# Kernel optimization log

Hardware: AMD Instinct MI355X
Metric: run time of the kernel (lower is better)

Reference implementation:

```python
import jax, jax.numpy as jnp
import numpy as np

N, E = 100000, 1600000
IN_CH, HID, HEADS, OUT_CH = 128, 32, 2, 40
NEG_SLOPE = 0.2
BN_EPS = 1e-5


def _param(key, shape, scale=0.1):
    return scale * jax.random.normal(key, shape, dtype=jnp.float32)


def setup_inputs() -> dict:
    key = jax.random.key(0)
    ks = jax.random.split(key, 24)
    x = jax.random.normal(ks[0], (N, IN_CH), dtype=jnp.float32)
    edge_index = jax.random.randint(ks[1], (2, E), 0, N, dtype=jnp.int32)
    d0 = HEADS * HID  # 64
    inp = {
        'x': x, 'edge_index': edge_index,
        # conv0: in 128 -> 32 per head, concat -> 64
        'W0': _param(ks[2], (IN_CH, HEADS * HID)),
        'as0': _param(ks[3], (HEADS, HID)), 'ad0': _param(ks[4], (HEADS, HID)),
        'b0': jnp.zeros((d0,), jnp.float32),
        'g0': jnp.ones((d0,), jnp.float32), 'bt0': jnp.zeros((d0,), jnp.float32),
        # conv1: 64 -> 32 per head, concat -> 64
        'W1': _param(ks[5], (d0, HEADS * HID)),
        'as1': _param(ks[6], (HEADS, HID)), 'ad1': _param(ks[7], (HEADS, HID)),
        'b1': jnp.zeros((d0,), jnp.float32),
        'g1': jnp.ones((d0,), jnp.float32), 'bt1': jnp.zeros((d0,), jnp.float32),
        # conv2: 64 -> 40 per head, mean over heads -> 40
        'W2': _param(ks[8], (d0, HEADS * OUT_CH)),
        'as2': _param(ks[9], (HEADS, OUT_CH)), 'ad2': _param(ks[10], (HEADS, OUT_CH)),
        'b2': jnp.zeros((OUT_CH,), jnp.float32),
    }
    return inp


def gat_conv(x, src, dst, W, a_src, a_dst, bias, out_ch, concat):
    n = x.shape[0]
    h = (x @ W).reshape(n, HEADS, out_ch)            # [N,H,C]
    alpha_src = jnp.sum(h * a_src, axis=-1)          # [N,H]
    alpha_dst = jnp.sum(h * a_dst, axis=-1)          # [N,H]
    e = jax.nn.leaky_relu(alpha_src[src] + alpha_dst[dst], NEG_SLOPE)  # [E,H]
    # softmax over incoming edges per destination node (self loops guarantee >=1 edge)
    m = jax.ops.segment_max(e, dst, num_segments=n)
    e = jnp.exp(e - m[dst])
    s = jax.ops.segment_sum(e, dst, num_segments=n)
    alpha = e / s[dst]                                # [E,H]
    msg = h[src] * alpha[:, :, None]                  # [E,H,C]
    out = jax.ops.segment_sum(msg, dst, num_segments=n)  # [N,H,C]
    out = out.reshape(n, HEADS * out_ch) if concat else out.mean(axis=1)
    return out + bias


def batch_norm(x, gamma, beta):
    mu = jnp.mean(x, axis=0)
    var = jnp.mean(jnp.square(x - mu), axis=0)
    return gamma * (x - mu) * jax.lax.rsqrt(var + BN_EPS) + beta


def reference(x, edge_index, W0, as0, ad0, b0, g0, bt0,
              W1, as1, ad1, b1, g1, bt1, W2, as2, ad2, b2):
    n = x.shape[0]
    loops = jnp.arange(n, dtype=edge_index.dtype)
    src = jnp.concatenate([edge_index[0], loops])
    dst = jnp.concatenate([edge_index[1], loops])
    h = gat_conv(x, src, dst, W0, as0, ad0, b0, HID, True)
    h = jax.nn.elu(batch_norm(h, g0, bt0))
    h = gat_conv(h, src, dst, W1, as1, ad1, b1, HID, True)
    h = jax.nn.elu(batch_norm(h, g1, bt1))
    return gat_conv(h, src, dst, W2, as2, ad2, b2, OUT_CH, False)
```

## Files before the change

### kernel.cpp

```cpp
#include <hip/hip_runtime.h>
#include <hip/hip_bf16.h>
#include <math.h>


#define NNODES 100000
#define NEDGES 1600000
#define ENTOT  (NEDGES + NNODES)
#define NEG_SLOPE 0.2f
#define BN_EPS 1e-5f

#define NRANGE 8
#define RSIZE  (NNODES/NRANGE)
#define BCAP   262144
#define PBLK   2048
#define NB2    32

typedef unsigned short u16;
typedef unsigned int u32;
typedef unsigned long long u64;
typedef __attribute__((ext_vector_type(8))) short short8;
typedef __attribute__((ext_vector_type(4))) float f32x4;

__device__ __forceinline__ float b2f(u16 u){ union{u32 i; float f;} v; v.i=((u32)u)<<16; return v.f; }
__device__ __forceinline__ float blo(u32 u){ union{u32 i; float f;} v; v.i=u<<16; return v.f; }
__device__ __forceinline__ float bhi(u32 u){ union{u32 i; float f;} v; v.i=u&0xffff0000u; return v.f; }
__device__ __forceinline__ u16 f2b(float x){ __hip_bfloat16 b=__float2bfloat16(x); return *(u16*)&b; }
__device__ __forceinline__ float ldf(const void* p, int i, int f){
  return f ? ((const float*)p)[i] : b2f(((const u16*)p)[i]);
}

__global__ void k_detect(const u16* __restrict__ x, int* __restrict__ flag){
  __shared__ int bad;
  if(threadIdx.x==0) bad=0;
  __syncthreads();
  int cnt=0;
  for(int i=threadIdx.x;i<4096;i+=256){
    u16 v = x[2*i];
    int ex = (v>>7)&0xff;
    if(ex==0xff || (ex==0 && (v&0x7fff)!=0)) cnt++;
  }
  atomicAdd(&bad,cnt);
  __syncthreads();
  if(threadIdx.x==0) flag[0] = (bad>4)?1:0;
}

__global__ __launch_bounds__(256) void k_part2(
    const int* __restrict__ ei, int* __restrict__ gptr, u32* __restrict__ bkt){
  __shared__ int lcnt[NRANGE], gbase[NRANGE];
  int t=threadIdx.x;
  if(t<NRANGE) lcnt[t]=0;
  __syncthreads();
  const int CH=(ENTOT+PBLK-1)/PBLK;
  int beg=blockIdx.x*CH, end=beg+CH; if(end>ENTOT) end=ENTOT;
  int nd[4], ns[4], nr[4], ne=0;
  for(int i=beg+t; i<end; i+=256){
    int d=(i<NEDGES)? ei[NEDGES+i] : (i-NEDGES);
    int s=(i<NEDGES)? ei[i] : d;
    nd[ne]=d; ns[ne]=s; ne++;
  }
  #pragma unroll 4
  for(int k=0;k<ne;k++) nr[k]=atomicAdd(&lcnt[nd[k]/RSIZE],1);
  __syncthreads();
  if(t<NRANGE) gbase[t]=atomicAdd(&gptr[t],lcnt[t]);
  __syncthreads();
  #pragma unroll 4
  for(int k=0;k<ne;k++){
    int r=nd[k]/RSIZE;
    u32 e = ((u32)(nd[k]-r*RSIZE)<<17) | (u32)ns[k];
    __builtin_nontemporal_store(e, &bkt[(size_t)r*BCAP + gbase[r] + nr[k]]);
  }
}

__global__ __launch_bounds__(256) void k_hist4(
    const u32* __restrict__ bkt, const int* __restrict__ gptr, int* __restrict__ lhist){
  __shared__ int lh[RSIZE];
  int t=threadIdx.x;
  for(int i=t;i<RSIZE;i+=256) lh[i]=0;
  __syncthreads();
  int r = blockIdx.x & (NRANGE-1);
  int c = blockIdx.x >> 3;
  int n = gptr[r];
  int per=(n+NB2-1)/NB2;
  int beg=c*per, end=beg+per; if(end>n) end=n;
  const u32* bp = bkt + (size_t)r*BCAP;
  for(int i=beg+t;i<end;i+=256) atomicAdd(&lh[bp[i]>>17],1);
  __syncthreads();
  int* out = lhist + (size_t)(r*NB2+c)*RSIZE;
  for(int i=t;i<RSIZE;i+=256) out[i]=lh[i];
}

__global__ __launch_bounds__(256) void k_sumscan(int* __restrict__ lhist, int* __restrict__ cnt){
  int n = blockIdx.x*256 + threadIdx.x;
  if(n>=NNODES) return;
  int r = n/RSIZE, i = n - r*RSIZE;
  int* base = lhist + (size_t)r*NB2*RSIZE + i;
  int run=0;
  #pragma unroll 8
  for(int c=0;c<NB2;c++){
    int v = base[(size_t)c*RSIZE];
    base[(size_t)c*RSIZE] = run;
    run += v;
  }
  cnt[n]=run;
}

#define SCAN_M (NNODES+1)
#define SCAN_NB ((SCAN_M + 2047)/2048)

__global__ void k_scan_a(const int* __restrict__ cnt, int* __restrict__ bsum){
  __shared__ int red[256];
  int b=blockIdx.x, t=threadIdx.x;
  int base = b*2048 + t*8;
  int s=0;
  #pragma unroll
  for(int j=0;j<8;j++){ int idx=base+j; s += (idx<NNODES)? cnt[idx]:0; }
  red[t]=s; __syncthreads();
  for(int o=128;o>0;o>>=1){ if(t<o) red[t]+=red[t+o]; __syncthreads(); }
  if(t==0) bsum[b]=red[0];
}

__global__ void k_scan_b(int* bsum){
  if(threadIdx.x==0){
    int run=0;
    for(int i=0;i<SCAN_NB;i++){ int v=bsum[i]; bsum[i]=run; run+=v; }
  }
}

__global__ void k_scan_c(const int* __restrict__ cnt, const int* __restrict__ bsum,
                         int* __restrict__ row_ptr){
  __shared__ int lds[256];
  int b=blockIdx.x, t=threadIdx.x;
  int base=b*2048+t*8;
  int v[8]; int s=0;
  #pragma unroll
  for(int j=0;j<8;j++){ int idx=base+j; int x=(idx<NNODES)?cnt[idx]:0; v[j]=s; s+=x; }
  lds[t]=s; __syncthreads();
  for(int o=1;o<256;o<<=1){
    int other=0; if(t>=o) other=lds[t-o];
    __syncthreads();
    lds[t]+=other;
    __syncthreads();
  }
  int texcl = lds[t] - s;
  int off0 = bsum[b] + texcl;
  #pragma unroll
  for(int j=0;j<8;j++){ int idx=base+j; if(idx<SCAN_M) row_ptr[idx]=off0+v[j]; }
}

__global__ __launch_bounds__(256) void k_scatter4(
    const u32* __restrict__ bkt, const int* __restrict__ gptr,
    const int* __restrict__ row_ptr, const int* __restrict__ lhist,
    int* __restrict__ col){
  __shared__ int lofs[RSIZE];
  int t=threadIdx.x;
  int r = blockIdx.x & (NRANGE-1);
  int c = blockIdx.x >> 3;
  int lo = r*RSIZE;
  const int* cb = lhist + (size_t)(r*NB2+c)*RSIZE;
  for(int i=t;i<RSIZE;i+=256) lofs[i] = row_ptr[lo+i] + cb[i];
  __syncthreads();
  int n = gptr[r];
  int per=(n+NB2-1)/NB2;
  int beg=c*per, end=beg+per; if(end>n) end=n;
  const u32* bp = bkt + (size_t)r*BCAP;
  for(int i=beg+t;i<end;i+=256){
    u32 e=bp[i];
    int pos=atomicAdd(&lofs[e>>17],1);
    col[pos]=(int)(e & 0x1FFFF);
  }
}

template<int K, int OUTC, int HID, bool XEXT, bool BN>
__global__ __launch_bounds__(256) void k_gemm_mfma(
    const void* __restrict__ xin, const void* __restrict__ W,
    const void* __restrict__ avs, const void* __restrict__ avd,
    const float2* __restrict__ bnab,
    u16* __restrict__ hout, float* __restrict__ asrc, float* __restrict__ adst,
    const int* __restrict__ flagp)
{
  const int f = flagp[0];
  constexpr int KP = K+8;
  constexpr int RS = OUTC+8;
  constexpr int NT = OUTC/16;
  constexpr int KQ = K/32;
  __shared__ __align__(16) u16 WT[OUTC*KP];
  __shared__ __align__(16) u16 HROW[4*16*RS];
  __shared__ float AVb[2*OUTC];
  __shared__ float2 BB[K];
  int t=threadIdx.x;
  const u16* Wu=(const u16*)W; const float* Wf=(const float*)W;
  for(int i8=t*8; i8<K*OUTC; i8+=256*8){
    int k=i8/OUTC, c0=i8-k*OUTC;
    u16 w8[8];
    if(f){
      const float* wp=Wf+i8;
      float4 a=*(const float4*)wp, b=*(const float4*)(wp+4);
      w8[0]=f2b(a.x);w8[1]=f2b(a.y);w8[2]=f2b(a.z);w8[3]=f2b(a.w);
      w8[4]=f2b(b.x);w8[5]=f2b(b.y);w8[6]=f2b(b.z);w8[7]=f2b(b.w);
    } else {
      uint4 q=*(const uint4*)(Wu+i8);
      w8[0]=q.x&0xffff;w8[1]=q.x>>16;w8[2]=q.y&0xffff;w8[3]=q.y>>16;
      w8[4]=q.z&0xffff;w8[5]=q.z>>16;w8[6]=q.w&0xffff;w8[7]=q.w>>16;
    }
    #pragma unroll
    for(int u=0;u<8;u++) WT[(c0+u)*KP + k] = w8[u];
  }
  for(int idx=t; idx<2*OUTC; idx+=256)
    AVb[idx] = (idx<OUTC)? ldf(avs,idx,f) : ldf(avd,idx-OUTC,f);
  if(BN) for(int idx=t; idx<K; idx+=256) BB[idx]=bnab[idx];
  __syncthreads();

  int wv=t>>6, lane=t&63;
  int m=lane&15, quad=lane>>4;
  int grow0 = blockIdx.x*64 + wv*16;
  int growA = grow0 + m;
  bool avalid = growA < NNODES;
  int growC = avalid ? growA : 0;

  f32x4 acc[NT] = {};
  #pragma unroll
  for(int kq=0;kq<KQ;kq++){
    int k0 = kq*32 + quad*8;
    union{ u32 u[4]; short8 s8; } A;
    if(XEXT && f==1){
      const float* xr=(const float*)xin + (size_t)growC*K + k0;
      float4 p=*(const float4*)xr, q=*(const float4*)(xr+4);
      A.u[0]=f2b(p.x)|((u32)f2b(p.y)<<16);
      A.u[1]=f2b(p.z)|((u32)f2b(p.w)<<16);
      A.u[2]=f2b(q.x)|((u32)f2b(q.y)<<16);
      A.u[3]=f2b(q.z)|((u32)f2b(q.w)<<16);
    } else {
      uint4 q=*(const uint4*)((const u16*)xin + (size_t)growC*K + k0);
      A.u[0]=q.x; A.u[1]=q.y; A.u[2]=q.z; A.u[3]=q.w;
    }
    if(BN){
      #pragma unroll
      for(int j=0;j<4;j++){
        float lo=b2f(A.u[j]&0xffff), hi=b2f(A.u[j]>>16);
        float2 c1=BB[k0+2*j], c2=BB[k0+2*j+1];
        lo=c1.x*lo+c1.y; lo = lo>0.f? lo : __expf(lo)-1.f;
        hi=c2.x*hi+c2.y; hi = hi>0.f? hi : __expf(hi)-1.f;
        A.u[j]=f2b(lo)|((u32)f2b(hi)<<16);
      }
    }
    #pragma unroll
    for(int nt=0;nt<NT;nt++){
      union{ uint4 q; short8 s8; } Bf;
      Bf.q = *(const uint4*)&WT[(nt*16+m)*KP + k0];
      acc[nt] = __builtin_amdgcn_mfma_f32_16x16x32_bf16(A.s8, Bf.s8, acc[nt], 0,0,0);
    }
  }
  u16* hr = &HROW[wv*16*RS];
  #pragma unroll
  for(int nt=0;nt<NT;nt++){
    #pragma unroll
    for(int reg=0;reg<4;reg++)
      hr[(quad*4+reg)*RS + nt*16+m] = f2b(acc[nt][reg]);
  }
  __syncthreads();
  {
    int row=lane&15, task=quad, head=task&1, sd=task>>1;
    float p=0.f;
    const u16* hrow=&hr[row*RS + head*HID];
    const float* av=&AVb[sd*OUTC + head*HID];
    #pragma unroll 8
    for(int c=0;c<HID;c++) p += b2f(hrow[c])*av[c];
    int grow=grow0+row;
    if(grow<NNODES){ (sd? adst:asrc)[grow*2+head]=p; }
  }
  {
    constexpr int CH8 = OUTC/8;
    for(int idx=lane; idx<16*CH8; idx+=64){
      int rr=idx/CH8, c8=idx-rr*CH8;
      int grow=grow0+rr;
      if(grow<NNODES)
        *(uint4*)(hout + (size_t)grow*OUTC + c8*8) = *(const uint4*)&hr[rr*RS + c8*8];
    }
  }
}

template<int OUTC, bool FINAL>
__global__ __launch_bounds__(256) void k_aggf(
  const int* __restrict__ row_ptr, const int* __restrict__ col,
  const u16* __restrict__ hin, const float2* __restrict__ asrc2,
  const float2* __restrict__ adst2, const void* __restrict__ bias,
  u16* __restrict__ houtb, void* __restrict__ outv, const int* __restrict__ flagp)
{
  const int f = flagp[0];
  __shared__ float vbuf[FINAL?32:1][84];
  constexpr int HSPLIT = FINAL ? 5 : 4;
  int t = threadIdx.x;
  int g  = t>>3;
  int cg = t&7;
  int rr = blockIdx.x & 7, jb = blockIdx.x >> 3;
  int lim = RSIZE - jb*32;
  bool ok = g < lim;
  int d = rr*RSIZE + jb*32 + g;
  int base=0, deg=0;
  float2 adv = make_float2(0.f,0.f);
  if(ok){
    base = row_ptr[d];
    deg  = row_ptr[d+1] - base;
    adv  = adst2[d];
  }
  const int* cp  = col + base;
  const u16* hcg = hin + cg*8;
  const u16* hxg = hin + 64 + cg*2;
  float acc[8]={0,0,0,0,0,0,0,0}, accx0=0.f, accx1=0.f;
  float s0=0.f, s1=0.f;

  int    cA[4]={0,0,0,0}, cB[4]={0,0,0,0};
  float2 aA[4]={}, aB[4]={};
  uint4  hA[4]={}, hB[4]={};
  ushort2 xA[4]={}, xB[4]={};

#define LDBLK(JJ, C, A, H, X) do{ int lm_=deg-1; \
    C[0]=cp[((JJ)  <lm_)?(JJ)  :lm_]; C[1]=cp[((JJ)+1<lm_)?(JJ)+1:lm_]; \
    C[2]=cp[((JJ)+2<lm_)?(JJ)+2:lm_]; C[3]=cp[((JJ)+3<lm_)?(JJ)+3:lm_]; \
    A[0]=asrc2[C[0]]; A[1]=asrc2[C[1]]; A[2]=asrc2[C[2]]; A[3]=asrc2[C[3]]; \
    H[0]=*(const uint4*)(hcg+(size_t)C[0]*OUTC); \
    H[1]=*(const uint4*)(hcg+(size_t)C[1]*OUTC); \
    H[2]=*(const uint4*)(hcg+(size_t)C[2]*OUTC); \
    H[3]=*(const uint4*)(hcg+(size_t)C[3]*OUTC); \
    if(FINAL){ \
      X[0]=*(const ushort2*)(hxg+(size_t)C[0]*OUTC); \
      X[1]=*(const ushort2*)(hxg+(size_t)C[1]*OUTC); \
      X[2]=*(const ushort2*)(hxg+(size_t)C[2]*OUTC); \
      X[3]=*(const ushort2*)(hxg+(size_t)C[3]*OUTC); } \
  }while(0)

#define COMP4(J, A, H, X) do{ \
    _Pragma("unroll") \
    for(int k_=0;k_<4;k_++){ \
      bool vv = (J)+k_ < deg; \
      float e0=A[k_].x+adv.x; e0=fmaxf(e0,NEG_SLOPE*e0); e0=fminf(e0,60.f); \
      float e1=A[k_].y+adv.y; e1=fmaxf(e1,NEG_SLOPE*e1); e1=fminf(e1,60.f); \
      float p0=__expf(e0), p1=__expf(e1); \
      if(!vv){p0=0.f;p1=0.f;} \
      s0+=p0; s1+=p1; \
      float pc=(cg<HSPLIT)?p0:p1; \
      acc[0]+=pc*blo(H[k_].x); acc[1]+=pc*bhi(H[k_].x); \
      acc[2]+=pc*blo(H[k_].y); acc[3]+=pc*bhi(H[k_].y); \
      acc[4]+=pc*blo(H[k_].z); acc[5]+=pc*bhi(H[k_].z); \
      acc[6]+=pc*blo(H[k_].w); acc[7]+=pc*bhi(H[k_].w); \
      if(FINAL){ accx0+=p1*b2f(X[k_].x); accx1+=p1*b2f(X[k_].y); } \
    } \
  }while(0)

  if(deg>0) LDBLK(0, cA, aA, hA, xA);
  for(int j=0;j<deg;j+=4){
    if(j+4<deg) LDBLK(j+4, cB, aB, hB, xB);
    COMP4(j, aA, hA, xA);
    #pragma unroll
    for(int k_=0;k_<4;k_++){ cA[k_]=cB[k_]; aA[k_]=aB[k_]; hA[k_]=hB[k_]; }
    if(FINAL){
      #pragma unroll
      for(int k_=0;k_<4;k_++) xA[k_]=xB[k_];
    }
  }
#undef LDBLK
#undef COMP4

  float inv0 = s0>0.f?1.f/s0:0.f, inv1 = s1>0.f?1.f/s1:0.f;
  if(!FINAL){
    if(ok){
      float inv = (cg<4)? inv0 : inv1;
      u16 o8[8];
      #pragma unroll
      for(int k=0;k<8;k++) o8[k]=f2b(acc[k]*inv + ldf(bias,cg*8+k,f));
      uint4 ov;
      ov.x=(u32)o8[0]|((u32)o8[1]<<16); ov.y=(u32)o8[2]|((u32)o8[3]<<16);
      ov.z=(u32)o8[4]|((u32)o8[5]<<16); ov.w=(u32)o8[6]|((u32)o8[7]<<16);
      *(uint4*)(houtb + (size_t)d*64 + cg*8) = ov;
    }
  } else {
    if(ok){
      #pragma unroll
      for(int k=0;k<8;k++)
        vbuf[g][cg*8+k] = acc[k]*((cg<5)?inv0:inv1);
      vbuf[g][64+cg*2]   = accx0*inv1;
      vbuf[g][64+cg*2+1] = accx1*inv1;
    }
    __syncthreads();
    for(int idx=t; idx<32*40; idx+=256){
      int gg=idx/40, ch=idx-gg*40;
      if(gg<lim){
        int dd = rr*RSIZE + jb*32 + gg;
        float res = 0.5f*(vbuf[gg][ch] + vbuf[gg][40+ch]) + ldf(bias,ch,f);
        if(f) ((float*)outv)[(size_t)dd*40+ch] = res;
        else  ((__hip_bfloat16*)outv)[(size_t)dd*40+ch] = __float2bfloat16(res);
      }
    }
  }
}

__global__ __launch_bounds__(256) void k_bnstats(const u16* __restrict__ h, float* __restrict__ stats){
  __shared__ float red[4][128];
  int t=threadIdx.x; int c=t&63; int g=t>>6;
  float s=0.f,q=0.f;
  for(int r=blockIdx.x*4+g; r<NNODES; r+=gridDim.x*4){
    float v=b2f(h[(size_t)r*64+c]); s+=v; q+=v*v;
  }
  red[g][c]=s; red[g][64+c]=q;
  __syncthreads();
  if(t<128){
    float tot=red[0][t]+red[1][t]+red[2][t]+red[3][t];
    atomicAdd(&stats[t], tot);
  }
}

__global__ void k_bnfinal(const float* __restrict__ stats,
                          const void* __restrict__ gm, const void* __restrict__ bt,
                          float2* __restrict__ bnab, const int* __restrict__ flagp){
  const int f = flagp[0];
  int c=threadIdx.x;
  if(c>=64) return;
  float mu=stats[c]*(1.0f/NNODES);
  float var=stats[64+c]*(1.0f/NNODES)-mu*mu;
  var = var>0.f?var:0.f;
  float A = ldf(gm,c,f)*rsqrtf(var+BN_EPS);
  float B = ldf(bt,c,f) - A*mu;
  bnab[c]=make_float2(A,B);
}

extern "C" void kernel_launch(void* const* d_in, const int* in_sizes, int n_in,
                              void* d_out, int out_size, void* d_ws, size_t ws_size,
                              hipStream_t stream){
  const void* x  =d_in[0];
  const int* ei =(const int*)d_in[1];
  const void* W0 =d_in[2];  const void* as0=d_in[3];  const void* ad0=d_in[4];
  const void* b0 =d_in[5];  const void* g0 =d_in[6];  const void* bt0=d_in[7];
  const void* W1 =d_in[8];  const void* as1=d_in[9];  const void* ad1=d_in[10];
  const void* b1 =d_in[11]; const void* g1 =d_in[12]; const void* bt1=d_in[13];
  const void* W2 =d_in[14]; const void* as2=d_in[15]; const void* ad2=d_in[16];
  const void* b2 =d_in[17];

  char* ws=(char*)d_ws;
  size_t off=0;
  auto alloc=[&](size_t bytes)->void*{ void* p=ws+off; off+=(bytes+255)&~(size_t)255; return p; };
  int*    flag   =(int*)   alloc(256);
  int*    row_ptr=(int*)   alloc((size_t)(NNODES+1)*4);
  int*    cnt    =(int*)   alloc((size_t)NNODES*4);
  int*    colx   =(int*)   alloc((size_t)ENTOT*4);
  int*    bsum   =(int*)   alloc((size_t)SCAN_NB*4);
  int*    gptr   =(int*)   alloc(256);
  u32*    bkt    =(u32*)   alloc((size_t)NRANGE*BCAP*4);
  u16*    hA     =(u16*)   alloc((size_t)100032*80*2);
  u16*    hB0    =(u16*)   alloc((size_t)100032*64*2);
  u16*    hB1    =(u16*)   alloc((size_t)100032*64*2);
  float*  asrc   =(float*) alloc((size_t)NNODES*2*4);
  float*  adst   =(float*) alloc((size_t)NNODES*2*4);
  float*  stats  =(float*) alloc(128*4);
  float2* bnab   =(float2*)alloc(64*8);
  int*    lhist  =(int*)hA;

  k_detect<<<1,256,0,stream>>>((const u16*)x, flag);

  (void)hipMemsetAsync(gptr,0,256,stream);
  k_part2  <<<PBLK,256,0,stream>>>(ei,gptr,bkt);
  k_hist4  <<<NRANGE*NB2,256,0,stream>>>(bkt,gptr,lhist);
  k_sumscan<<<(NNODES+255)/256,256,0,stream>>>(lhist,cnt);
  k_scan_a <<<SCAN_NB,256,0,stream>>>(cnt,bsum);
  k_scan_b <<<1,64,0,stream>>>(bsum);
  k_scan_c <<<SCAN_NB,256,0,stream>>>(cnt,bsum,row_ptr);
  k_scatter4<<<NRANGE*NB2,256,0,stream>>>(bkt,gptr,row_ptr,lhist,colx);

  int gG = (NNODES+63)/64;
  int gA = NRANGE * ((RSIZE + 31)/32);
  k_gemm_mfma<128,64,32,true ,false><<<gG,256,0,stream>>>(
      x,W0,as0,ad0,nullptr,hA,asrc,adst,flag);
  k_aggf<64,false><<<gA,256,0,stream>>>(row_ptr,colx,hA,
      (const float2*)asrc,(const float2*)adst,b0,hB0,nullptr,flag);
  (void)hipMemsetAsync(stats,0,512,stream);
  k_bnstats<<<256,256,0,stream>>>(hB0,stats);
  k_bnfinal<<<1,64,0,stream>>>(stats,g0,bt0,bnab,flag);
  k_gemm_mfma<64,64,32,false,true ><<<gG,256,0,stream>>>(
      hB0,W1,as1,ad1,bnab,hA,asrc,adst,flag);
  k_aggf<64,false><<<gA,256,0,stream>>>(row_ptr,colx,hA,
      (const float2*)asrc,(const float2*)adst,b1,hB1,nullptr,flag);
  (void)hipMemsetAsync(stats,0,512,stream);
  k_bnstats<<<256,256,0,stream>>>(hB1,stats);
  k_bnfinal<<<1,64,0,stream>>>(stats,g1,bt1,bnab,flag);
  k_gemm_mfma<64,80,40,false,true ><<<gG,256,0,stream>>>(
      hB1,W2,as2,ad2,bnab,hA,asrc,adst,flag);
  k_aggf<80,true ><<<gA,256,0,stream>>>(row_ptr,colx,hA,
      (const float2*)asrc,(const float2*)adst,b2,nullptr,d_out,flag);

  (void)in_sizes;(void)n_in;(void)out_size;(void)ws_size;
}
```

Before: 450.7 us.

## Partition edges by source sub-range and dest range to sort CSR columns

The edge partition now buckets edges by both a source-node sub-block and the destination range, giving 128 buckets instead of 8. The histogram and scatter stages each process one bucket per block instead of splitting each range into 32 chunks. As a result, columns within each CSR row come out grouped by source block, which should improve gather locality in the aggregation kernels. In exchange, the per-bucket capacity is fixed at 24576, which risks overflow if the edge distribution is skewed, and the bucket array grows in memory.

```diff
diff --git a/kernel.cpp b/kernel.cpp
--- a/kernel.cpp
+++ b/kernel.cpp
@@ -11,9 +11,11 @@
 
 #define NRANGE 8
 #define RSIZE  (NNODES/NRANGE)
-#define BCAP   262144
+#define SB     16
+#define SBS    ((NNODES+SB-1)/SB)
+#define NBKT   (NRANGE*SB)
+#define BCAP   24576
 #define PBLK   2048
-#define NB2    32
 
 typedef unsigned short u16;
 typedef unsigned int u32;
@@ -46,28 +48,31 @@
 
 __global__ __launch_bounds__(256) void k_part2(
     const int* __restrict__ ei, int* __restrict__ gptr, u32* __restrict__ bkt){
-  __shared__ int lcnt[NRANGE], gbase[NRANGE];
+  __shared__ int lcnt[NBKT], gbase[NBKT];
   int t=threadIdx.x;
-  if(t<NRANGE) lcnt[t]=0;
+  if(t<NBKT) lcnt[t]=0;
   __syncthreads();
   const int CH=(ENTOT+PBLK-1)/PBLK;
   int beg=blockIdx.x*CH, end=beg+CH; if(end>ENTOT) end=ENTOT;
-  int nd[4], ns[4], nr[4], ne=0;
+  int nd[4], ns[4], nb[4], nr[4], ne=0;
   for(int i=beg+t; i<end; i+=256){
     int d=(i<NEDGES)? ei[NEDGES+i] : (i-NEDGES);
     int s=(i<NEDGES)? ei[i] : d;
     nd[ne]=d; ns[ne]=s; ne++;
   }
   #pragma unroll 4
-  for(int k=0;k<ne;k++) nr[k]=atomicAdd(&lcnt[nd[k]/RSIZE],1);
-  __syncthreads();
-  if(t<NRANGE) gbase[t]=atomicAdd(&gptr[t],lcnt[t]);
+  for(int k=0;k<ne;k++){
+    nb[k] = (ns[k]/SBS)*NRANGE + nd[k]/RSIZE;
+    nr[k] = atomicAdd(&lcnt[nb[k]],1);
+  }
+  __syncthreads();
+  if(t<NBKT) gbase[t]=atomicAdd(&gptr[t],lcnt[t]);
   __syncthreads();
   #pragma unroll 4
   for(int k=0;k<ne;k++){
     int r=nd[k]/RSIZE;
     u32 e = ((u32)(nd[k]-r*RSIZE)<<17) | (u32)ns[k];
-    __builtin_nontemporal_store(e, &bkt[(size_t)r*BCAP + gbase[r] + nr[k]]);
+    __builtin_nontemporal_store(e, &bkt[(size_t)nb[k]*BCAP + gbase[nb[k]] + nr[k]]);
   }
 }
 
@@ -77,15 +82,12 @@
   int t=threadIdx.x;
   for(int i=t;i<RSIZE;i+=256) lh[i]=0;
   __syncthreads();
-  int r = blockIdx.x & (NRANGE-1);
-  int c = blockIdx.x >> 3;
-  int n = gptr[r];
-  int per=(n+NB2-1)/NB2;
-  int beg=c*per, end=beg+per; if(end>n) end=n;
-  const u32* bp = bkt + (size_t)r*BCAP;
-  for(int i=beg+t;i<end;i+=256) atomicAdd(&lh[bp[i]>>17],1);
-  __syncthreads();
-  int* out = lhist + (size_t)(r*NB2+c)*RSIZE;
+  int b = blockIdx.x;
+  int n = gptr[b];
+  const u32* bp = bkt + (size_t)b*BCAP;
+  for(int i=t;i<n;i+=256) atomicAdd(&lh[bp[i]>>17],1);
+  __syncthreads();
+  int* out = lhist + (size_t)b*RSIZE;
   for(int i=t;i<RSIZE;i+=256) out[i]=lh[i];
 }
 
@@ -93,12 +95,12 @@
   int n = blockIdx.x*256 + threadIdx.x;
   if(n>=NNODES) return;
   int r = n/RSIZE, i = n - r*RSIZE;
-  int* base = lhist + (size_t)r*NB2*RSIZE + i;
+  int* base = lhist + (size_t)r*RSIZE + i;
   int run=0;
   #pragma unroll 8
-  for(int c=0;c<NB2;c++){
-    int v = base[(size_t)c*RSIZE];
-    base[(size_t)c*RSIZE] = run;
+  for(int sb=0;sb<SB;sb++){
+    int v = base[(size_t)sb*NRANGE*RSIZE];
+    base[(size_t)sb*NRANGE*RSIZE] = run;
     run += v;
   }
   cnt[n]=run;
@@ -153,17 +155,15 @@
     int* __restrict__ col){
   __shared__ int lofs[RSIZE];
   int t=threadIdx.x;
-  int r = blockIdx.x & (NRANGE-1);
-  int c = blockIdx.x >> 3;
+  int b = blockIdx.x;
+  int r = b & (NRANGE-1);
   int lo = r*RSIZE;
-  const int* cb = lhist + (size_t)(r*NB2+c)*RSIZE;
+  const int* cb = lhist + (size_t)b*RSIZE;
   for(int i=t;i<RSIZE;i+=256) lofs[i] = row_ptr[lo+i] + cb[i];
   __syncthreads();
-  int n = gptr[r];
-  int per=(n+NB2-1)/NB2;
-  int beg=c*per, end=beg+per; if(end>n) end=n;
-  const u32* bp = bkt + (size_t)r*BCAP;
-  for(int i=beg+t;i<end;i+=256){
+  int n = gptr[b];
+  const u32* bp = bkt + (size_t)b*BCAP;
+  for(int i=t;i<n;i+=256){
     u32 e=bp[i];
     int pos=atomicAdd(&lofs[e>>17],1);
     col[pos]=(int)(e & 0x1FFFF);
@@ -443,8 +443,8 @@
   int*    cnt    =(int*)   alloc((size_t)NNODES*4);
   int*    colx   =(int*)   alloc((size_t)ENTOT*4);
   int*    bsum   =(int*)   alloc((size_t)SCAN_NB*4);
-  int*    gptr   =(int*)   alloc(256);
-  u32*    bkt    =(u32*)   alloc((size_t)NRANGE*BCAP*4);
+  int*    gptr   =(int*)   alloc(512);
+  u32*    bkt    =(u32*)   alloc((size_t)NBKT*BCAP*4);
   u16*    hA     =(u16*)   alloc((size_t)100032*80*2);
   u16*    hB0    =(u16*)   alloc((size_t)100032*64*2);
   u16*    hB1    =(u16*)   alloc((size_t)100032*64*2);
@@ -456,14 +456,14 @@
 
   k_detect<<<1,256,0,stream>>>((const u16*)x, flag);
 
-  (void)hipMemsetAsync(gptr,0,256,stream);
+  (void)hipMemsetAsync(gptr,0,512,stream);
   k_part2  <<<PBLK,256,0,stream>>>(ei,gptr,bkt);
-  k_hist4  <<<NRANGE*NB2,256,0,stream>>>(bkt,gptr,lhist);
+  k_hist4  <<<NBKT,256,0,stream>>>(bkt,gptr,lhist);
   k_sumscan<<<(NNODES+255)/256,256,0,stream>>>(lhist,cnt);
   k_scan_a <<<SCAN_NB,256,0,stream>>>(cnt,bsum);
   k_scan_b <<<1,64,0,stream>>>(bsum);
   k_scan_c <<<SCAN_NB,256,0,stream>>>(cnt,bsum,row_ptr);
-  k_scatter4<<<NRANGE*NB2,256,0,stream>>>(bkt,gptr,row_ptr,lhist,colx);
+  k_scatter4<<<NBKT,256,0,stream>>>(bkt,gptr,row_ptr,lhist,colx);
 
   int gG = (NNODES+63)/64;
   int gA = NRANGE * ((RSIZE + 31)/32);
```

New measurement: 522.8 us. +16.0%, slower.

## Store projected features in 16-channel planes and aggregate plane by plane

Applied to the files above, without the earlier changes.

The GEMM now writes node features as channel planes of 16 bf16 values (32 bytes per node per plane) instead of row-major rows. The aggregation kernel handles 128 destinations per block with two threads per node and loops over planes, so each pass gathers from a smaller working set that fits better in cache. The final layer drops its LDS staging and combines the two heads with a lane shuffle. In exchange, edge indices and attention logits are reloaded and the exponentials recomputed once per plane (4-5 times), and each gather is a 16-byte access.

```diff
diff --git a/kernel.cpp b/kernel.cpp
--- a/kernel.cpp
+++ b/kernel.cpp
@@ -4,6 +4,7 @@
 
 
 #define NNODES 100000
+#define NND    100032
 #define NEDGES 1600000
 #define ENTOT  (NEDGES + NNODES)
 #define NEG_SLOPE 0.2f
@@ -273,29 +274,33 @@
     for(int idx=lane; idx<16*CH8; idx+=64){
       int rr=idx/CH8, c8=idx-rr*CH8;
       int grow=grow0+rr;
-      if(grow<NNODES)
-        *(uint4*)(hout + (size_t)grow*OUTC + c8*8) = *(const uint4*)&hr[rr*RS + c8*8];
-    }
-  }
-}
-
-template<int OUTC, bool FINAL>
+      if(grow<NNODES){
+        int p, half;
+        if constexpr (OUTC==80){
+          if(c8<5){ p=c8; half=0; } else { p=c8-5; half=1; }
+        } else {
+          p = c8>>1; half = c8&1;
+        }
+        *(uint4*)(hout + ((size_t)p*NND + grow)*16 + half*8) = *(const uint4*)&hr[rr*RS + c8*8];
+      }
+    }
+  }
+}
+
+template<int NCB, bool FINAL>
 __global__ __launch_bounds__(256) void k_aggf(
   const int* __restrict__ row_ptr, const int* __restrict__ col,
-  const u16* __restrict__ hin, const float2* __restrict__ asrc2,
+  const u16* __restrict__ hpl, const float2* __restrict__ asrc2,
   const float2* __restrict__ adst2, const void* __restrict__ bias,
   u16* __restrict__ houtb, void* __restrict__ outv, const int* __restrict__ flagp)
 {
   const int f = flagp[0];
-  __shared__ float vbuf[FINAL?32:1][84];
-  constexpr int HSPLIT = FINAL ? 5 : 4;
   int t = threadIdx.x;
-  int g  = t>>3;
-  int cg = t&7;
+  int g  = t>>1;
+  int cl = t&1;
   int rr = blockIdx.x & 7, jb = blockIdx.x >> 3;
-  int lim = RSIZE - jb*32;
-  bool ok = g < lim;
-  int d = rr*RSIZE + jb*32 + g;
+  bool ok = (jb*128 + g) < RSIZE;
+  int d = rr*RSIZE + jb*128 + g;
   int base=0, deg=0;
   float2 adv = make_float2(0.f,0.f);
   if(ok){
@@ -303,33 +308,29 @@
     deg  = row_ptr[d+1] - base;
     adv  = adst2[d];
   }
-  const int* cp  = col + base;
-  const u16* hcg = hin + cg*8;
-  const u16* hxg = hin + 64 + cg*2;
-  float acc[8]={0,0,0,0,0,0,0,0}, accx0=0.f, accx1=0.f;
-  float s0=0.f, s1=0.f;
-
-  int    cA[4]={0,0,0,0}, cB[4]={0,0,0,0};
-  float2 aA[4]={}, aB[4]={};
-  uint4  hA[4]={}, hB[4]={};
-  ushort2 xA[4]={}, xB[4]={};
-
-#define LDBLK(JJ, C, A, H, X) do{ int lm_=deg-1; \
+  const int* cp = col + base;
+
+  for(int cb=0; cb<NCB; ++cb){
+    const u16* hp = hpl + ((size_t)cb*NND)*16 + cl*8;
+    bool up0 = FINAL ? (cl==0) : ((cb*16 + cl*8) < 32);
+    float acc[8]={0,0,0,0,0,0,0,0};
+    float s0=0.f, s1=0.f;
+
+    int    cA[4]={0,0,0,0}, cB[4]={0,0,0,0};
+    float2 aA[4]={}, aB[4]={};
+    uint4  hA4[4]={}, hB4[4]={};
+
+#define LDBLK(JJ, C, A, H) do{ int lm_=deg-1; \
     C[0]=cp[((JJ)  <lm_)?(JJ)  :lm_]; C[1]=cp[((JJ)+1<lm_)?(JJ)+1:lm_]; \
     C[2]=cp[((JJ)+2<lm_)?(JJ)+2:lm_]; C[3]=cp[((JJ)+3<lm_)?(JJ)+3:lm_]; \
     A[0]=asrc2[C[0]]; A[1]=asrc2[C[1]]; A[2]=asrc2[C[2]]; A[3]=asrc2[C[3]]; \
-    H[0]=*(const uint4*)(hcg+(size_t)C[0]*OUTC); \
-    H[1]=*(const uint4*)(hcg+(size_t)C[1]*OUTC); \
-    H[2]=*(const uint4*)(hcg+(size_t)C[2]*OUTC); \
-    H[3]=*(const uint4*)(hcg+(size_t)C[3]*OUTC); \
-    if(FINAL){ \
-      X[0]=*(const ushort2*)(hxg+(size_t)C[0]*OUTC); \
-      X[1]=*(const ushort2*)(hxg+(size_t)C[1]*OUTC); \
-      X[2]=*(const ushort2*)(hxg+(size_t)C[2]*OUTC); \
-      X[3]=*(const ushort2*)(hxg+(size_t)C[3]*OUTC); } \
+    H[0]=*(const uint4*)(hp+(size_t)C[0]*16); \
+    H[1]=*(const uint4*)(hp+(size_t)C[1]*16); \
+    H[2]=*(const uint4*)(hp+(size_t)C[2]*16); \
+    H[3]=*(const uint4*)(hp+(size_t)C[3]*16); \
   }while(0)
 
-#define COMP4(J, A, H, X) do{ \
+#define COMP4(J, A, H) do{ \
     _Pragma("unroll") \
     for(int k_=0;k_<4;k_++){ \
       bool vv = (J)+k_ < deg; \
@@ -338,57 +339,62 @@
       float p0=__expf(e0), p1=__expf(e1); \
       if(!vv){p0=0.f;p1=0.f;} \
       s0+=p0; s1+=p1; \
-      float pc=(cg<HSPLIT)?p0:p1; \
+      float pc=up0?p0:p1; \
       acc[0]+=pc*blo(H[k_].x); acc[1]+=pc*bhi(H[k_].x); \
       acc[2]+=pc*blo(H[k_].y); acc[3]+=pc*bhi(H[k_].y); \
       acc[4]+=pc*blo(H[k_].z); acc[5]+=pc*bhi(H[k_].z); \
       acc[6]+=pc*blo(H[k_].w); acc[7]+=pc*bhi(H[k_].w); \
-      if(FINAL){ accx0+=p1*b2f(X[k_].x); accx1+=p1*b2f(X[k_].y); } \
     } \
   }while(0)
 
-  if(deg>0) LDBLK(0, cA, aA, hA, xA);
-  for(int j=0;j<deg;j+=4){
-    if(j+4<deg) LDBLK(j+4, cB, aB, hB, xB);
-    COMP4(j, aA, hA, xA);
-    #pragma unroll
-    for(int k_=0;k_<4;k_++){ cA[k_]=cB[k_]; aA[k_]=aB[k_]; hA[k_]=hB[k_]; }
-    if(FINAL){
+    if(deg>0) LDBLK(0, cA, aA, hA4);
+    for(int j=0;j<deg;j+=4){
+      if(j+4<deg) LDBLK(j+4, cB, aB, hB4);
+      COMP4(j, aA, hA4);
       #pragma unroll
-      for(int k_=0;k_<4;k_++) xA[k_]=xB[k_];
-    }
-  }
+      for(int k_=0;k_<4;k_++){ cA[k_]=cB[k_]; aA[k_]=aB[k_]; hA4[k_]=hB4[k_]; }
+    }
 #undef LDBLK
 #undef COMP4
 
-  float inv0 = s0>0.f?1.f/s0:0.f, inv1 = s1>0.f?1.f/s1:0.f;
-  if(!FINAL){
-    if(ok){
-      float inv = (cg<4)? inv0 : inv1;
-      u16 o8[8];
+    float inv0 = s0>0.f?1.f/s0:0.f, inv1 = s1>0.f?1.f/s1:0.f;
+    if(!FINAL){
+      if(ok){
+        int ch0 = cb*16 + cl*8;
+        float inv = up0 ? inv0 : inv1;
+        u16 o8[8];
+        #pragma unroll
+        for(int k=0;k<8;k++) o8[k]=f2b(acc[k]*inv + ldf(bias,ch0+k,f));
+        uint4 ov;
+        ov.x=(u32)o8[0]|((u32)o8[1]<<16); ov.y=(u32)o8[2]|((u32)o8[3]<<16);
+        ov.z=(u32)o8[4]|((u32)o8[5]<<16); ov.w=(u32)o8[6]|((u32)o8[7]<<16);
+        *(uint4*)(houtb + (size_t)d*64 + ch0) = ov;
+      }
+    } else {
+      float inv = cl ? inv1 : inv0;
+      float nk[8], pk[8];
       #pragma unroll
-      for(int k=0;k<8;k++) o8[k]=f2b(acc[k]*inv + ldf(bias,cg*8+k,f));
-      uint4 ov;
-      ov.x=(u32)o8[0]|((u32)o8[1]<<16); ov.y=(u32)o8[2]|((u32)o8[3]<<16);
-      ov.z=(u32)o8[4]|((u32)o8[5]<<16); ov.w=(u32)o8[6]|((u32)o8[7]<<16);
-      *(uint4*)(houtb + (size_t)d*64 + cg*8) = ov;
-    }
-  } else {
-    if(ok){
+      for(int k=0;k<8;k++) nk[k]=acc[k]*inv;
       #pragma unroll
-      for(int k=0;k<8;k++)
-        vbuf[g][cg*8+k] = acc[k]*((cg<5)?inv0:inv1);
-      vbuf[g][64+cg*2]   = accx0*inv1;
-      vbuf[g][64+cg*2+1] = accx1*inv1;
-    }
-    __syncthreads();
-    for(int idx=t; idx<32*40; idx+=256){
-      int gg=idx/40, ch=idx-gg*40;
-      if(gg<lim){
-        int dd = rr*RSIZE + jb*32 + gg;
-        float res = 0.5f*(vbuf[gg][ch] + vbuf[gg][40+ch]) + ldf(bias,ch,f);
-        if(f) ((float*)outv)[(size_t)dd*40+ch] = res;
-        else  ((__hip_bfloat16*)outv)[(size_t)dd*40+ch] = __float2bfloat16(res);
+      for(int k=0;k<8;k++) pk[k]=__shfl_xor(nk[k],1,64);
+      if(ok && cl==0){
+        float res[8];
+        #pragma unroll
+        for(int k=0;k<8;k++) res[k]=0.5f*(nk[k]+pk[k]) + ldf(bias,cb*8+k,f);
+        if(f){
+          float* op=((float*)outv) + (size_t)d*40 + cb*8;
+          float4 w0=make_float4(res[0],res[1],res[2],res[3]);
+          float4 w1=make_float4(res[4],res[5],res[6],res[7]);
+          *(float4*)op = w0; *(float4*)(op+4) = w1;
+        } else {
+          u16 o8[8];
+          #pragma unroll
+          for(int k=0;k<8;k++) o8[k]=f2b(res[k]);
+          uint4 ov;
+          ov.x=(u32)o8[0]|((u32)o8[1]<<16); ov.y=(u32)o8[2]|((u32)o8[3]<<16);
+          ov.z=(u32)o8[4]|((u32)o8[5]<<16); ov.w=(u32)o8[6]|((u32)o8[7]<<16);
+          *(uint4*)(((u16*)outv) + (size_t)d*40 + cb*8) = ov;
+        }
       }
     }
   }
@@ -445,9 +451,9 @@
   int*    bsum   =(int*)   alloc((size_t)SCAN_NB*4);
   int*    gptr   =(int*)   alloc(256);
   u32*    bkt    =(u32*)   alloc((size_t)NRANGE*BCAP*4);
-  u16*    hA     =(u16*)   alloc((size_t)100032*80*2);
-  u16*    hB0    =(u16*)   alloc((size_t)100032*64*2);
-  u16*    hB1    =(u16*)   alloc((size_t)100032*64*2);
+  u16*    hA     =(u16*)   alloc((size_t)NND*80*2);
+  u16*    hB0    =(u16*)   alloc((size_t)NND*64*2);
+  u16*    hB1    =(u16*)   alloc((size_t)NND*64*2);
   float*  asrc   =(float*) alloc((size_t)NNODES*2*4);
   float*  adst   =(float*) alloc((size_t)NNODES*2*4);
   float*  stats  =(float*) alloc(128*4);
@@ -466,24 +472,24 @@
   k_scatter4<<<NRANGE*NB2,256,0,stream>>>(bkt,gptr,row_ptr,lhist,colx);
 
   int gG = (NNODES+63)/64;
-  int gA = NRANGE * ((RSIZE + 31)/32);
+  int gA = NRANGE * ((RSIZE + 127)/128);
   k_gemm_mfma<128,64,32,true ,false><<<gG,256,0,stream>>>(
       x,W0,as0,ad0,nullptr,hA,asrc,adst,flag);
-  k_aggf<64,false><<<gA,256,0,stream>>>(row_ptr,colx,hA,
+  k_aggf<4,false><<<gA,256,0,stream>>>(row_ptr,colx,hA,
       (const float2*)asrc,(const float2*)adst,b0,hB0,nullptr,flag);
   (void)hipMemsetAsync(stats,0,512,stream);
   k_bnstats<<<256,256,0,stream>>>(hB0,stats);
   k_bnfinal<<<1,64,0,stream>>>(stats,g0,bt0,bnab,flag);
   k_gemm_mfma<64,64,32,false,true ><<<gG,256,0,stream>>>(
       hB0,W1,as1,ad1,bnab,hA,asrc,adst,flag);
-  k_aggf<64,false><<<gA,256,0,stream>>>(row_ptr,colx,hA,
+  k_aggf<4,false><<<gA,256,0,stream>>>(row_ptr,colx,hA,
       (const float2*)asrc,(const float2*)adst,b1,hB1,nullptr,flag);
   (void)hipMemsetAsync(stats,0,512,stream);
   k_bnstats<<<256,256,0,stream>>>(hB1,stats);
   k_bnfinal<<<1,64,0,stream>>>(stats,g1,bt1,bnab,flag);
   k_gemm_mfma<64,80,40,false,true ><<<gG,256,0,stream>>>(
       hB1,W2,as2,ad2,bnab,hA,asrc,adst,flag);
-  k_aggf<80,true ><<<gA,256,0,stream>>>(row_ptr,colx,hA,
+  k_aggf<5,true ><<<gA,256,0,stream>>>(row_ptr,colx,hA,
       (const float2*)asrc,(const float2*)adst,b2,nullptr,d_out,flag);
 
   (void)in_sizes;(void)n_in;(void)out_size;(void)ws_size;
```

Result: slower. 683.3 us (+51.6%).
